# Optimization experiments

Hardware: AMD Instinct MI355X
Metric: run time of the kernel (lower is better)

The kernel has to match this reference:

```python
import jax, jax.numpy as jnp
import numpy as np

NUM_HEADS = 12

def setup_inputs() -> dict:
    key = jax.random.key(0)
    ks = jax.random.split(key, 6)
    B, N, C = 8, 1024, 768
    x = jax.random.normal(ks[0], (B, N, C), dtype=jnp.float32)
    qkv_w = jax.random.normal(ks[1], (3 * C, C), dtype=jnp.float32) * 0.02
    qkv_b = jax.random.normal(ks[2], (3 * C,), dtype=jnp.float32) * 0.02
    static_a = jax.random.normal(ks[3], (1, NUM_HEADS, N, N), dtype=jnp.float32) * 0.02
    proj_w = jax.random.normal(ks[4], (C, C), dtype=jnp.float32) * 0.02
    proj_b = jax.random.normal(ks[5], (C,), dtype=jnp.float32) * 0.02
    return {"x": x, "qkv_w": qkv_w, "qkv_b": qkv_b, "static_a": static_a,
            "proj_w": proj_w, "proj_b": proj_b}

def reference(x, qkv_w, qkv_b, static_a, proj_w, proj_b):
    B, N, C = x.shape
    H = NUM_HEADS
    D = C // H
    scale = D ** -0.5
    # qkv: [B,N,3C] -> [3,B,H,N,D]
    qkv = (x @ qkv_w.T + qkv_b).reshape(B, N, 3, H, D).transpose(2, 0, 3, 1, 4)
    q, k, v = qkv[0], qkv[1], qkv[2]
    attn = jnp.einsum('bhnd,bhmd->bhnm', q, k) * scale
    attn = jax.nn.softmax(attn, axis=-1)
    attn = attn + static_a  # static bias added AFTER softmax (no renorm)
    out = jnp.einsum('bhnm,bhmd->bhnd', attn, v)  # [B,H,N,D]
    out = out.transpose(0, 2, 1, 3).reshape(B, N, C)
    return out @ proj_w.T + proj_b
```

## Files before the change

kernel.cpp:

```cpp
#include <hip/hip_runtime.h>
#include <math.h>

#define NB   8
#define SEQ  1024
#define CH   768
#define NH   12
#define HD   64
#define BHT  (NB * NH)
#define QKVN 2304

typedef unsigned short u16;
typedef unsigned int   u32;
typedef __attribute__((ext_vector_type(8))) short bf16x8;
typedef __attribute__((ext_vector_type(4))) float f32x4;

__device__ __forceinline__ float bf2f(u32 s) {
    union { u32 u; float f; } v; v.u = s << 16; return v.f;
}
__device__ __forceinline__ u16 f2bf(float f) {
    union { float f; u32 u; } v; v.f = f;
    u32 u = v.u;
    return (u16)((u + 0x7fffu + ((u >> 16) & 1u)) >> 16);
}
__device__ __forceinline__ float ld1(const u16* p) { return bf2f((u32)*p); }
__device__ __forceinline__ void st4v(u16* p, float a, float b, float c, float d) {
    ushort4 o; o.x = f2bf(a); o.y = f2bf(b); o.z = f2bf(c); o.w = f2bf(d);
    *(ushort4*)p = o;
}
__device__ __forceinline__ void st4v(float* p, float a, float b, float c, float d) {
    float4 o; o.x = a; o.y = b; o.z = c; o.w = d;
    *(float4*)p = o;
}
__device__ __forceinline__ void gload16(const u16* g, u16* l) {
    __builtin_amdgcn_global_load_lds(
        (const __attribute__((address_space(1))) void*)g,
        (__attribute__((address_space(3))) void*)l, 16, 0, 0);
}

__global__ void detect_kernel(const u32* __restrict__ x, int* __restrict__ flag) {
    __shared__ int cnt;
    if (threadIdx.x == 0) cnt = 0;
    __syncthreads();
    int c = 0;
    for (int i = threadIdx.x; i < 2048; i += 256) {
        const u32 e0 = (x[i] >> 7) & 0xFFu;
        c += (e0 >= 110u && e0 <= 132u) ? 1 : 0;
    }
    atomicAdd(&cnt, c);
    __syncthreads();
    if (threadIdx.x == 0) *flag = (cnt > 1024) ? 1 : 0;
}

#define PREP_V4 5309184
__device__ __forceinline__ void prep_seg(size_t v, const size_t e0[6],
                                         int* segp, size_t* offp) {
    int seg = 5;
    if      (v < 1572864) seg = 0;
    else if (v < 2015232) seg = 1;
    else if (v < 2015808) seg = 2;
    else if (v < 5161536) seg = 3;
    else if (v < 5308992) seg = 4;
    *segp = seg; *offp = v * 4 - e0[seg];
}

__global__ __launch_bounds__(256) void prep_all(
    const int* __restrict__ flag,
    const void* __restrict__ s0, const void* __restrict__ s1, const void* __restrict__ s2,
    const void* __restrict__ s3, const void* __restrict__ s4, const void* __restrict__ s5,
    u16* __restrict__ dst)
{
    const size_t e0[6] = {0, 6291456, 8060928, 8063232, 20646144, 21235968};
    if (*flag != 0) {
        const u16* const srcs[6] = {(const u16*)s0, (const u16*)s1, (const u16*)s2,
                                    (const u16*)s3, (const u16*)s4, (const u16*)s5};
        for (size_t v = blockIdx.x * 256 + threadIdx.x; v < PREP_V4; v += (size_t)gridDim.x * 256) {
            int seg; size_t off;
            prep_seg(v, e0, &seg, &off);
            *(ushort4*)(dst + v * 4) = *(const ushort4*)(srcs[seg] + off);
        }
    } else {
        const float* const srcs[6] = {(const float*)s0, (const float*)s1, (const float*)s2,
                                      (const float*)s3, (const float*)s4, (const float*)s5};
        for (size_t v = blockIdx.x * 256 + threadIdx.x; v < PREP_V4; v += (size_t)gridDim.x * 256) {
            int seg; size_t off;
            prep_seg(v, e0, &seg, &off);
            const float4 f = *(const float4*)(srcs[seg] + off);
            ushort4 o; o.x = f2bf(f.x); o.y = f2bf(f.y); o.z = f2bf(f.z); o.w = f2bf(f.w);
            *(ushort4*)(dst + v * 4) = o;
        }
    }
}

template<bool SWAP>
__device__ __forceinline__ void gemm128_core(
    const u16* __restrict__ Ag, const u16* __restrict__ Bg,
    f32x4 acc[4][4], u16* As, u16* Bs, int wm, int wn, int l15, int quad)
{
    const int t = threadIdx.x;
    const int w = t >> 6, lane = t & 63;
    const int lr = lane >> 2, lc = lane & 3;
    const int r0 = w * 16 + lr;
    const int r1 = 64 + w * 16 + lr;
    const int g0 = (lc + r0) & 3, g1 = (lc + r1) & 3;
    const u16* a0 = Ag + (size_t)r0 * CH + g0 * 8;
    const u16* a1 = Ag + (size_t)r1 * CH + g1 * 8;
    const u16* b0 = Bg + (size_t)r0 * CH + g0 * 8;
    const u16* b1 = Bg + (size_t)r1 * CH + g1 * 8;
    u16* lA0 = As + w * 512;
    u16* lA1 = As + 2048 + w * 512;
    u16* lB0 = Bs + w * 512;
    u16* lB1 = Bs + 2048 + w * 512;

#pragma unroll
    for (int mi = 0; mi < 4; mi++)
#pragma unroll
        for (int ni = 0; ni < 4; ni++) { f32x4 z = {0.f,0.f,0.f,0.f}; acc[mi][ni] = z; }

    for (int k0 = 0; k0 < CH; k0 += 32) {
        __syncthreads();
        gload16(a0 + k0, lA0);
        gload16(a1 + k0, lA1);
        gload16(b0 + k0, lB0);
        gload16(b1 + k0, lB1);
        __syncthreads();
        bf16x8 af[4], bfr[4];
#pragma unroll
        for (int mi = 0; mi < 4; mi++) {
            const int ra = wm * 64 + mi * 16 + l15;
            af[mi] = *(const bf16x8*)&As[ra * 32 + ((quad - ra) & 3) * 8];
        }
#pragma unroll
        for (int ni = 0; ni < 4; ni++) {
            const int rb = wn * 64 + ni * 16 + l15;
            bfr[ni] = *(const bf16x8*)&Bs[rb * 32 + ((quad - rb) & 3) * 8];
        }
#pragma unroll
        for (int mi = 0; mi < 4; mi++)
#pragma unroll
            for (int ni = 0; ni < 4; ni++)
                acc[mi][ni] = SWAP
                    ? __builtin_amdgcn_mfma_f32_16x16x32_bf16(bfr[ni], af[mi], acc[mi][ni], 0, 0, 0)
                    : __builtin_amdgcn_mfma_f32_16x16x32_bf16(af[mi], bfr[ni], acc[mi][ni], 0, 0, 0);
    }
}

template<bool SWAP>
__device__ __forceinline__ void gemm128x64_core(
    const u16* __restrict__ Ag, const u16* __restrict__ Bg,
    f32x4 acc[4][2], u16* As, u16* Bs, int wm, int wn, int l15, int quad)
{
    const int t = threadIdx.x;
    const int w = t >> 6, lane = t & 63;
    const int lr = lane >> 2, lc = lane & 3;
    const int r0 = w * 16 + lr;
    const int r1 = 64 + w * 16 + lr;
    const int g0 = (lc + r0) & 3, g1 = (lc + r1) & 3;
    const u16* a0 = Ag + (size_t)r0 * CH + g0 * 8;
    const u16* a1 = Ag + (size_t)r1 * CH + g1 * 8;
    const u16* b0 = Bg + (size_t)r0 * CH + g0 * 8;
    u16* lA0 = As + w * 512;
    u16* lA1 = As + 2048 + w * 512;
    u16* lB0 = Bs + w * 512;

#pragma unroll
    for (int mi = 0; mi < 4; mi++)
#pragma unroll
        for (int ni = 0; ni < 2; ni++) { f32x4 z = {0.f,0.f,0.f,0.f}; acc[mi][ni] = z; }

    for (int k0 = 0; k0 < CH; k0 += 32) {
        __syncthreads();
        gload16(a0 + k0, lA0);
        gload16(a1 + k0, lA1);
        gload16(b0 + k0, lB0);
        __syncthreads();
        bf16x8 af[4], bfr[2];
#pragma unroll
        for (int mi = 0; mi < 4; mi++) {
            const int ra = wm * 64 + mi * 16 + l15;
            af[mi] = *(const bf16x8*)&As[ra * 32 + ((quad - ra) & 3) * 8];
        }
#pragma unroll
        for (int ni = 0; ni < 2; ni++) {
            const int rb = wn * 32 + ni * 16 + l15;
            bfr[ni] = *(const bf16x8*)&Bs[rb * 32 + ((quad - rb) & 3) * 8];
        }
#pragma unroll
        for (int mi = 0; mi < 4; mi++)
#pragma unroll
            for (int ni = 0; ni < 2; ni++)
                acc[mi][ni] = SWAP
                    ? __builtin_amdgcn_mfma_f32_16x16x32_bf16(bfr[ni], af[mi], acc[mi][ni], 0, 0, 0)
                    : __builtin_amdgcn_mfma_f32_16x16x32_bf16(af[mi], bfr[ni], acc[mi][ni], 0, 0, 0);
    }
}

__global__ __launch_bounds__(256) void qkv_gemm(
    const u16* __restrict__ x, const u16* __restrict__ w, const u16* __restrict__ bias,
    u16* __restrict__ Qn, u16* __restrict__ Kn, u16* __restrict__ Vt)
{
    __shared__ u16 As[128 * 32];
    __shared__ u16 Bs[128 * 32];
    const int id  = blockIdx.y * 18 + blockIdx.x;
    const int xcd = id & 7, seq0 = id >> 3;
    const int by  = xcd * 8 + seq0 / 18;
    const int bx  = seq0 % 18;
    const int t = threadIdx.x, lane = t & 63, wv = t >> 6;
    const int l15 = lane & 15, quad = lane >> 4;
    const int wm = wv >> 1, wn = wv & 1;
    const int m0 = by * 128, n0 = bx * 128;
    const int which = n0 / CH;
    const int h     = ((n0 % CH) >> 6) + wn;
    const int b     = m0 >> 10;
    const size_t bh = (size_t)b * NH + h;
    const int sq0   = m0 & 1023;
    f32x4 acc[4][4];

    if (which == 2) {
        gemm128_core<false>(x + (size_t)m0 * CH, w + (size_t)n0 * CH,
                            acc, As, Bs, wm, wn, l15, quad);
        float bv[4];
#pragma unroll
        for (int ni = 0; ni < 4; ni++) bv[ni] = ld1(bias + n0 + wn * 64 + ni * 16 + l15);
#pragma unroll
        for (int mi = 0; mi < 4; mi++) {
            const int seq = sq0 + wm * 64 + mi * 16 + quad * 4;
#pragma unroll
            for (int ni = 0; ni < 4; ni++) {
                const int d = ni * 16 + l15;
                st4v(&Vt[(bh * HD + d) * SEQ + seq],
                     acc[mi][ni][0] + bv[ni], acc[mi][ni][1] + bv[ni],
                     acc[mi][ni][2] + bv[ni], acc[mi][ni][3] + bv[ni]);
            }
        }
    } else {
        gemm128_core<true>(x + (size_t)m0 * CH, w + (size_t)n0 * CH,
                           acc, As, Bs, wm, wn, l15, quad);
        u16* T2 = which ? Kn : Qn;
        const float qsc = which ? 1.0f : 0.125f;
        float bvr[4][4];
#pragma unroll
        for (int ni = 0; ni < 4; ni++)
#pragma unroll
            for (int r = 0; r < 4; r++)
                bvr[ni][r] = ld1(bias + n0 + wn * 64 + ni * 16 + quad * 4 + r);
#pragma unroll
        for (int mi = 0; mi < 4; mi++) {
            const int seq = sq0 + wm * 64 + mi * 16 + l15;
#pragma unroll
            for (int ni = 0; ni < 4; ni++) {
                const int dbase = ni * 16 + quad * 4;
                st4v(&T2[(bh * SEQ + seq) * HD + dbase],
                     (acc[mi][ni][0] + bvr[ni][0]) * qsc,
                     (acc[mi][ni][1] + bvr[ni][1]) * qsc,
                     (acc[mi][ni][2] + bvr[ni][2]) * qsc,
                     (acc[mi][ni][3] + bvr[ni][3]) * qsc);
            }
        }
    }
}

__global__ __launch_bounds__(256) void attn_kernel(
    const u16* __restrict__ Qn, const u16* __restrict__ Kn, const u16* __restrict__ Vt,
    const u16* __restrict__ Ab, u16* __restrict__ AO)
{
    __shared__ u16 Ks[64 * 72];
    __shared__ u16 Vs[64 * 72];
    __shared__ u16 Ps[4 * 32 * 72];

    const int qb = blockIdx.x;
    const int y  = blockIdx.y;
    const int hh = y >> 3, b = y & 7;
    const size_t bh = (size_t)b * NH + hh;
    const int t  = threadIdx.x;
    const int w  = t >> 6, lane = t & 63;
    const int l15 = lane & 15, quad = lane >> 4;
    const int sr = t >> 2, sc = (t & 3) * 16;
    const int i0g = qb * 128 + w * 32;
    u16* Psw = Ps + w * 32 * 72;

    bf16x8 qa[2][2];
#pragma unroll
    for (int isub = 0; isub < 2; isub++)
#pragma unroll
        for (int db = 0; db < 2; db++)
            qa[isub][db] = *(const bf16x8*)(Qn +
                (bh * SEQ + i0g + isub * 16 + l15) * HD + db * 32 + quad * 8);

    f32x4 Op[2][4], Oa[2][4];
#pragma unroll
    for (int i = 0; i < 2; i++)
#pragma unroll
        for (int d = 0; d < 4; d++) { f32x4 z = {0.f,0.f,0.f,0.f}; Op[i][d] = z; Oa[i][d] = z; }
    float rl[2][4] = {{0.f,0.f,0.f,0.f},{0.f,0.f,0.f,0.f}};

    for (int kt = 0; kt < 16; kt++) {
        const int j0 = kt * 64;
        bf16x8 afr[2][2];
#pragma unroll
        for (int jb = 0; jb < 2; jb++)
#pragma unroll
            for (int isub = 0; isub < 2; isub++)
                afr[jb][isub] = *(const bf16x8*)(Ab +
                    ((size_t)hh * SEQ + i0g + isub * 16 + l15) * SEQ
                    + j0 + jb * 32 + quad * 8);

        const u16* kp = Kn + (bh * SEQ + j0 + sr) * HD + sc;
        const u16* vp = Vt + (bh * HD + sr) * SEQ + j0 + sc;
        const uint4 k0v = *(const uint4*)kp, k1v = *(const uint4*)(kp + 8);
        const uint4 v0v = *(const uint4*)vp, v1v = *(const uint4*)(vp + 8);
        __syncthreads();
        *(uint4*)&Ks[sr * 72 + sc] = k0v; *(uint4*)&Ks[sr * 72 + sc + 8] = k1v;
        *(uint4*)&Vs[sr * 72 + sc] = v0v; *(uint4*)&Vs[sr * 72 + sc + 8] = v1v;
        __syncthreads();

#pragma unroll
        for (int j16 = 0; j16 < 4; j16++) {
            const bf16x8 kf0 = *(const bf16x8*)&Ks[(j16 * 16 + l15) * 72 + quad * 8];
            const bf16x8 kf1 = *(const bf16x8*)&Ks[(j16 * 16 + l15) * 72 + 32 + quad * 8];
#pragma unroll
            for (int isub = 0; isub < 2; isub++) {
                f32x4 s = {0.f, 0.f, 0.f, 0.f};
                s = __builtin_amdgcn_mfma_f32_16x16x32_bf16(qa[isub][0], kf0, s, 0, 0, 0);
                s = __builtin_amdgcn_mfma_f32_16x16x32_bf16(qa[isub][1], kf1, s, 0, 0, 0);
#pragma unroll
                for (int r = 0; r < 4; r++) {
                    const float p = __expf(fminf(s[r], 60.f));
                    rl[isub][r] += p;
                    Psw[(isub * 16 + quad * 4 + r) * 72 + j16 * 16 + l15] = f2bf(p);
                }
            }
        }

#pragma unroll
        for (int jb = 0; jb < 2; jb++) {
            bf16x8 pf[2];
#pragma unroll
            for (int isub = 0; isub < 2; isub++)
                pf[isub] = *(const bf16x8*)&Psw[(isub * 16 + l15) * 72 + jb * 32 + quad * 8];
#pragma unroll
            for (int d16 = 0; d16 < 4; d16++) {
                const bf16x8 vf = *(const bf16x8*)&Vs[(d16 * 16 + l15) * 72 + jb * 32 + quad * 8];
#pragma unroll
                for (int isub = 0; isub < 2; isub++) {
                    Op[isub][d16] = __builtin_amdgcn_mfma_f32_16x16x32_bf16(vf, pf[isub], Op[isub][d16], 0, 0, 0);
                    Oa[isub][d16] = __builtin_amdgcn_mfma_f32_16x16x32_bf16(vf, afr[jb][isub], Oa[isub][d16], 0, 0, 0);
                }
            }
        }
    }

    float inv[2];
#pragma unroll
    for (int isub = 0; isub < 2; isub++) {
        float rr[4];
#pragma unroll
        for (int r = 0; r < 4; r++) {
            float v = rl[isub][r];
            v += __shfl_xor(v, 1); v += __shfl_xor(v, 2);
            v += __shfl_xor(v, 4); v += __shfl_xor(v, 8);
            rr[r] = v;
        }
        const int src = (l15 >> 2) << 4;
        const float t0 = __shfl(rr[0], src), t1 = __shfl(rr[1], src);
        const float t2 = __shfl(rr[2], src), t3 = __shfl(rr[3], src);
        const float sel = (l15 & 2) ? ((l15 & 1) ? t3 : t2)
                                    : ((l15 & 1) ? t1 : t0);
        inv[isub] = 1.f / sel;
    }
#pragma unroll
    for (int isub = 0; isub < 2; isub++) {
        const int n = i0g + isub * 16 + l15;
#pragma unroll
        for (int d16 = 0; d16 < 4; d16++)
            st4v(&AO[((size_t)b * SEQ + n) * CH + hh * HD + d16 * 16 + quad * 4],
                 Op[isub][d16][0] * inv[isub] + Oa[isub][d16][0],
                 Op[isub][d16][1] * inv[isub] + Oa[isub][d16][1],
                 Op[isub][d16][2] * inv[isub] + Oa[isub][d16][2],
                 Op[isub][d16][3] * inv[isub] + Oa[isub][d16][3]);
    }
}

__global__ __launch_bounds__(256) void proj_all(
    const int* __restrict__ flag,
    const u16* __restrict__ AO, const u16* __restrict__ w, const u16* __restrict__ bias,
    void* __restrict__ outv)
{
    __shared__ u16 As[128 * 32];
    __shared__ u16 Bs[64 * 32];
    const int isbf = *flag;
    const int id  = blockIdx.y * 12 + blockIdx.x;
    const int xcd = id & 7, seq0 = id >> 3;
    const int by  = xcd * 8 + seq0 / 12;
    const int bx  = seq0 % 12;
    const int t = threadIdx.x, lane = t & 63, wv = t >> 6;
    const int l15 = lane & 15, quad = lane >> 4;
    const int wm = wv >> 1, wn = wv & 1;
    const int m0 = by * 128, n0 = bx * 64;

    f32x4 acc[4][2];
    gemm128x64_core<true>(AO + (size_t)m0 * CH, w + (size_t)n0 * CH,
                          acc, As, Bs, wm, wn, l15, quad);

    float bvr[2][4];
#pragma unroll
    for (int ni = 0; ni < 2; ni++)
#pragma unroll
        for (int r = 0; r < 4; r++)
            bvr[ni][r] = ld1(bias + n0 + wn * 32 + ni * 16 + quad * 4 + r);
#pragma unroll
    for (int mi = 0; mi < 4; mi++) {
        const int m = m0 + wm * 64 + mi * 16 + l15;
#pragma unroll
        for (int ni = 0; ni < 2; ni++) {
            const int n = n0 + wn * 32 + ni * 16 + quad * 4;
            if (isbf)
                st4v((u16*)outv + (size_t)m * CH + n,
                     acc[mi][ni][0] + bvr[ni][0], acc[mi][ni][1] + bvr[ni][1],
                     acc[mi][ni][2] + bvr[ni][2], acc[mi][ni][3] + bvr[ni][3]);
            else
                st4v((float*)outv + (size_t)m * CH + n,
                     acc[mi][ni][0] + bvr[ni][0], acc[mi][ni][1] + bvr[ni][1],
                     acc[mi][ni][2] + bvr[ni][2], acc[mi][ni][3] + bvr[ni][3]);
        }
    }
}

extern "C" void kernel_launch(void* const* d_in, const int* in_sizes, int n_in,
                              void* d_out, int out_size, void* d_ws, size_t ws_size,
                              hipStream_t stream) {
    (void)in_sizes; (void)n_in; (void)out_size; (void)ws_size;
    u16* ws = (u16*)d_ws;
    u16* xb   = ws;
    u16* wqb  = ws + 6291456;
    u16* bqb  = ws + 8060928;
    u16* Ab   = ws + 8063232;
    u16* pwb  = ws + 20646144;
    u16* pbb  = ws + 21235968;
    u16* arena_end = ws + 21236736;
    const size_t S1 = (size_t)NB * NH * SEQ * HD;
    u16* Qn = arena_end;
    u16* Kn = Qn + S1;
    u16* Vt = Kn + S1;
    u16* AO = Vt + S1;
    int* flag = (int*)(AO + S1);

    detect_kernel<<<dim3(1), dim3(256), 0, stream>>>((const u32*)d_in[0], flag);

    const dim3 blk(256);
    prep_all<<<dim3(4096), blk, 0, stream>>>(flag,
        d_in[0], d_in[1], d_in[2], d_in[3], d_in[4], d_in[5], ws);

    qkv_gemm<<<dim3(QKVN / 128, (NB * SEQ) / 128), blk, 0, stream>>>(
        xb, wqb, bqb, Qn, Kn, Vt);
    attn_kernel<<<dim3(SEQ / 128, BHT), blk, 0, stream>>>(Qn, Kn, Vt, Ab, AO);

    proj_all<<<dim3(CH / 64, (NB * SEQ) / 128), blk, 0, stream>>>(
        flag, AO, pwb, pbb, d_out);
}
```

Measured before the change: 271.0 us.

## Widen GEMM K-step to 64 and fold dtype detection into kernels

The QKV and projection GEMM cores now stage 64-wide K slices in LDS, using an 8-chunk XOR-style swizzle, and run two MFMA sub-steps per barrier pair. This halves the number of sync/load rounds per tile. Separately, the standalone detect kernel is removed: each block of prep_all and proj_all recomputes the bf16/fp32 detection from the input, which saves a launch and a dependency but adds a small redundant read per block. LDS usage doubles, which may reduce occupancy.

```diff
diff --git a/kernel.cpp b/kernel.cpp
--- a/kernel.cpp
+++ b/kernel.cpp
@@ -37,18 +37,18 @@
         (__attribute__((address_space(3))) void*)l, 16, 0, 0);
 }
 
-__global__ void detect_kernel(const u32* __restrict__ x, int* __restrict__ flag) {
-    __shared__ int cnt;
-    if (threadIdx.x == 0) cnt = 0;
+__device__ __forceinline__ int block_detect(const u32* __restrict__ x) {
+    __shared__ int cnt_;
+    if (threadIdx.x == 0) cnt_ = 0;
     __syncthreads();
     int c = 0;
     for (int i = threadIdx.x; i < 2048; i += 256) {
         const u32 e0 = (x[i] >> 7) & 0xFFu;
         c += (e0 >= 110u && e0 <= 132u) ? 1 : 0;
     }
-    atomicAdd(&cnt, c);
+    atomicAdd(&cnt_, c);
     __syncthreads();
-    if (threadIdx.x == 0) *flag = (cnt > 1024) ? 1 : 0;
+    return cnt_ > 1024 ? 1 : 0;
 }
 
 #define PREP_V4 5309184
@@ -64,13 +64,13 @@
 }
 
 __global__ __launch_bounds__(256) void prep_all(
-    const int* __restrict__ flag,
     const void* __restrict__ s0, const void* __restrict__ s1, const void* __restrict__ s2,
     const void* __restrict__ s3, const void* __restrict__ s4, const void* __restrict__ s5,
     u16* __restrict__ dst)
 {
     const size_t e0[6] = {0, 6291456, 8060928, 8063232, 20646144, 21235968};
-    if (*flag != 0) {
+    const int isbf = block_detect((const u32*)s0);
+    if (isbf) {
         const u16* const srcs[6] = {(const u16*)s0, (const u16*)s1, (const u16*)s2,
                                     (const u16*)s3, (const u16*)s4, (const u16*)s5};
         for (size_t v = blockIdx.x * 256 + threadIdx.x; v < PREP_V4; v += (size_t)gridDim.x * 256) {
@@ -98,49 +98,53 @@
 {
     const int t = threadIdx.x;
     const int w = t >> 6, lane = t & 63;
-    const int lr = lane >> 2, lc = lane & 3;
-    const int r0 = w * 16 + lr;
-    const int r1 = 64 + w * 16 + lr;
-    const int g0 = (lc + r0) & 3, g1 = (lc + r1) & 3;
-    const u16* a0 = Ag + (size_t)r0 * CH + g0 * 8;
-    const u16* a1 = Ag + (size_t)r1 * CH + g1 * 8;
-    const u16* b0 = Bg + (size_t)r0 * CH + g0 * 8;
-    const u16* b1 = Bg + (size_t)r1 * CH + g1 * 8;
-    u16* lA0 = As + w * 512;
-    u16* lA1 = As + 2048 + w * 512;
-    u16* lB0 = Bs + w * 512;
-    u16* lB1 = Bs + 2048 + w * 512;
+    const int lr = lane >> 3;
+    const int lc = lane & 7;
+    const int gch = ((lc + lr) & 7) * 8;
+    const u16* aP[4]; const u16* bP[4]; u16* lA[4]; u16* lB[4];
+#pragma unroll
+    for (int i = 0; i < 4; i++) {
+        const int r = i * 32 + w * 8 + lr;
+        aP[i] = Ag + (size_t)r * CH + gch;
+        bP[i] = Bg + (size_t)r * CH + gch;
+        lA[i] = As + (i * 32 + w * 8) * 64;
+        lB[i] = Bs + (i * 32 + w * 8) * 64;
+    }
 
 #pragma unroll
     for (int mi = 0; mi < 4; mi++)
 #pragma unroll
         for (int ni = 0; ni < 4; ni++) { f32x4 z = {0.f,0.f,0.f,0.f}; acc[mi][ni] = z; }
 
-    for (int k0 = 0; k0 < CH; k0 += 32) {
-        __syncthreads();
-        gload16(a0 + k0, lA0);
-        gload16(a1 + k0, lA1);
-        gload16(b0 + k0, lB0);
-        gload16(b1 + k0, lB1);
-        __syncthreads();
-        bf16x8 af[4], bfr[4];
-#pragma unroll
-        for (int mi = 0; mi < 4; mi++) {
-            const int ra = wm * 64 + mi * 16 + l15;
-            af[mi] = *(const bf16x8*)&As[ra * 32 + ((quad - ra) & 3) * 8];
-        }
-#pragma unroll
-        for (int ni = 0; ni < 4; ni++) {
-            const int rb = wn * 64 + ni * 16 + l15;
-            bfr[ni] = *(const bf16x8*)&Bs[rb * 32 + ((quad - rb) & 3) * 8];
-        }
-#pragma unroll
-        for (int mi = 0; mi < 4; mi++)
-#pragma unroll
-            for (int ni = 0; ni < 4; ni++)
-                acc[mi][ni] = SWAP
-                    ? __builtin_amdgcn_mfma_f32_16x16x32_bf16(bfr[ni], af[mi], acc[mi][ni], 0, 0, 0)
-                    : __builtin_amdgcn_mfma_f32_16x16x32_bf16(af[mi], bfr[ni], acc[mi][ni], 0, 0, 0);
+    for (int k0 = 0; k0 < CH; k0 += 64) {
+        __syncthreads();
+#pragma unroll
+        for (int i = 0; i < 4; i++) {
+            gload16(aP[i] + k0, lA[i]);
+            gload16(bP[i] + k0, lB[i]);
+        }
+        __syncthreads();
+#pragma unroll
+        for (int kk = 0; kk < 2; kk++) {
+            bf16x8 af[4], bfr[4];
+#pragma unroll
+            for (int mi = 0; mi < 4; mi++) {
+                const int ra = wm * 64 + mi * 16 + l15;
+                af[mi] = *(const bf16x8*)&As[ra * 64 + ((kk * 4 + quad - ra) & 7) * 8];
+            }
+#pragma unroll
+            for (int ni = 0; ni < 4; ni++) {
+                const int rb = wn * 64 + ni * 16 + l15;
+                bfr[ni] = *(const bf16x8*)&Bs[rb * 64 + ((kk * 4 + quad - rb) & 7) * 8];
+            }
+#pragma unroll
+            for (int mi = 0; mi < 4; mi++)
+#pragma unroll
+                for (int ni = 0; ni < 4; ni++)
+                    acc[mi][ni] = SWAP
+                        ? __builtin_amdgcn_mfma_f32_16x16x32_bf16(bfr[ni], af[mi], acc[mi][ni], 0, 0, 0)
+                        : __builtin_amdgcn_mfma_f32_16x16x32_bf16(af[mi], bfr[ni], acc[mi][ni], 0, 0, 0);
+        }
     }
 }
 
@@ -151,46 +155,56 @@
 {
     const int t = threadIdx.x;
     const int w = t >> 6, lane = t & 63;
-    const int lr = lane >> 2, lc = lane & 3;
-    const int r0 = w * 16 + lr;
-    const int r1 = 64 + w * 16 + lr;
-    const int g0 = (lc + r0) & 3, g1 = (lc + r1) & 3;
-    const u16* a0 = Ag + (size_t)r0 * CH + g0 * 8;
-    const u16* a1 = Ag + (size_t)r1 * CH + g1 * 8;
-    const u16* b0 = Bg + (size_t)r0 * CH + g0 * 8;
-    u16* lA0 = As + w * 512;
-    u16* lA1 = As + 2048 + w * 512;
-    u16* lB0 = Bs + w * 512;
+    const int lr = lane >> 3, lc = lane & 7;
+    const int gch = ((lc + lr) & 7) * 8;
+    const u16* aP[4]; u16* lA[4];
+    const u16* bP[2]; u16* lB[2];
+#pragma unroll
+    for (int i = 0; i < 4; i++) {
+        const int r = i * 32 + w * 8 + lr;
+        aP[i] = Ag + (size_t)r * CH + gch;
+        lA[i] = As + (i * 32 + w * 8) * 64;
+    }
+#pragma unroll
+    for (int i = 0; i < 2; i++) {
+        const int r = i * 32 + w * 8 + lr;
+        bP[i] = Bg + (size_t)r * CH + gch;
+        lB[i] = Bs + (i * 32 + w * 8) * 64;
+    }
 
 #pragma unroll
     for (int mi = 0; mi < 4; mi++)
 #pragma unroll
         for (int ni = 0; ni < 2; ni++) { f32x4 z = {0.f,0.f,0.f,0.f}; acc[mi][ni] = z; }
 
-    for (int k0 = 0; k0 < CH; k0 += 32) {
-        __syncthreads();
-        gload16(a0 + k0, lA0);
-        gload16(a1 + k0, lA1);
-        gload16(b0 + k0, lB0);
-        __syncthreads();
-        bf16x8 af[4], bfr[2];
-#pragma unroll
-        for (int mi = 0; mi < 4; mi++) {
-            const int ra = wm * 64 + mi * 16 + l15;
-            af[mi] = *(const bf16x8*)&As[ra * 32 + ((quad - ra) & 3) * 8];
-        }
-#pragma unroll
-        for (int ni = 0; ni < 2; ni++) {
-            const int rb = wn * 32 + ni * 16 + l15;
-            bfr[ni] = *(const bf16x8*)&Bs[rb * 32 + ((quad - rb) & 3) * 8];
-        }
-#pragma unroll
-        for (int mi = 0; mi < 4; mi++)
-#pragma unroll
-            for (int ni = 0; ni < 2; ni++)
-                acc[mi][ni] = SWAP
-                    ? __builtin_amdgcn_mfma_f32_16x16x32_bf16(bfr[ni], af[mi], acc[mi][ni], 0, 0, 0)
-                    : __builtin_amdgcn_mfma_f32_16x16x32_bf16(af[mi], bfr[ni], acc[mi][ni], 0, 0, 0);
+    for (int k0 = 0; k0 < CH; k0 += 64) {
+        __syncthreads();
+#pragma unroll
+        for (int i = 0; i < 4; i++) gload16(aP[i] + k0, lA[i]);
+#pragma unroll
+        for (int i = 0; i < 2; i++) gload16(bP[i] + k0, lB[i]);
+        __syncthreads();
+#pragma unroll
+        for (int kk = 0; kk < 2; kk++) {
+            bf16x8 af[4], bfr[2];
+#pragma unroll
+            for (int mi = 0; mi < 4; mi++) {
+                const int ra = wm * 64 + mi * 16 + l15;
+                af[mi] = *(const bf16x8*)&As[ra * 64 + ((kk * 4 + quad - ra) & 7) * 8];
+            }
+#pragma unroll
+            for (int ni = 0; ni < 2; ni++) {
+                const int rb = wn * 32 + ni * 16 + l15;
+                bfr[ni] = *(const bf16x8*)&Bs[rb * 64 + ((kk * 4 + quad - rb) & 7) * 8];
+            }
+#pragma unroll
+            for (int mi = 0; mi < 4; mi++)
+#pragma unroll
+                for (int ni = 0; ni < 2; ni++)
+                    acc[mi][ni] = SWAP
+                        ? __builtin_amdgcn_mfma_f32_16x16x32_bf16(bfr[ni], af[mi], acc[mi][ni], 0, 0, 0)
+                        : __builtin_amdgcn_mfma_f32_16x16x32_bf16(af[mi], bfr[ni], acc[mi][ni], 0, 0, 0);
+        }
     }
 }
 
@@ -198,8 +212,8 @@
     const u16* __restrict__ x, const u16* __restrict__ w, const u16* __restrict__ bias,
     u16* __restrict__ Qn, u16* __restrict__ Kn, u16* __restrict__ Vt)
 {
-    __shared__ u16 As[128 * 32];
-    __shared__ u16 Bs[128 * 32];
+    __shared__ u16 As[128 * 64];
+    __shared__ u16 Bs[128 * 64];
     const int id  = blockIdx.y * 18 + blockIdx.x;
     const int xcd = id & 7, seq0 = id >> 3;
     const int by  = xcd * 8 + seq0 / 18;
@@ -381,13 +395,13 @@
 }
 
 __global__ __launch_bounds__(256) void proj_all(
-    const int* __restrict__ flag,
+    const u32* __restrict__ xdet,
     const u16* __restrict__ AO, const u16* __restrict__ w, const u16* __restrict__ bias,
     void* __restrict__ outv)
 {
-    __shared__ u16 As[128 * 32];
-    __shared__ u16 Bs[64 * 32];
-    const int isbf = *flag;
+    __shared__ u16 As[128 * 64];
+    __shared__ u16 Bs[64 * 64];
+    const int isbf = block_detect(xdet);
     const int id  = blockIdx.y * 12 + blockIdx.x;
     const int xcd = id & 7, seq0 = id >> 3;
     const int by  = xcd * 8 + seq0 / 12;
@@ -442,12 +456,9 @@
     u16* Kn = Qn + S1;
     u16* Vt = Kn + S1;
     u16* AO = Vt + S1;
-    int* flag = (int*)(AO + S1);
-
-    detect_kernel<<<dim3(1), dim3(256), 0, stream>>>((const u32*)d_in[0], flag);
 
     const dim3 blk(256);
-    prep_all<<<dim3(4096), blk, 0, stream>>>(flag,
+    prep_all<<<dim3(4096), blk, 0, stream>>>(
         d_in[0], d_in[1], d_in[2], d_in[3], d_in[4], d_in[5], ws);
 
     qkv_gemm<<<dim3(QKVN / 128, (NB * SEQ) / 128), blk, 0, stream>>>(
@@ -455,5 +466,5 @@
     attn_kernel<<<dim3(SEQ / 128, BHT), blk, 0, stream>>>(Qn, Kn, Vt, Ab, AO);
 
     proj_all<<<dim3(CH / 64, (NB * SEQ) / 128), blk, 0, stream>>>(
-        flag, AO, pwb, pbb, d_out);
-}
+        (const u32*)d_in[0], AO, pwb, pbb, d_out);
+}
```

Result: no change. 271.6 us (+0.2%).
